# Kernel tuning notes

Measured on AMD Instinct MI355X. Metric: run time of the kernel, lower is better.

## Reference

```python
import jax, jax.numpy as jnp
import numpy as np

EPS_MASK = 1e-6   # clamp eps from DNN_Beamformer __init__
EPS_MVDR = 1e-15  # eps in get_mvdr_vector / psd normalization
SCALING = 2.0     # AttentionReference softmax scaling


def _psd(xs, mask):
    # xs: (B,F,C,T) complex, mask: (B,F,C,T) real -> psd: (B,F,C,C) complex
    m = mask.mean(axis=-2)                                   # (B,F,T)
    m = m / (m.sum(axis=-1, keepdims=True) + EPS_MVDR)
    # sum_t xs[c,t] * conj(xs[e,t]) * m[t], never materializing (B,F,T,C,C)
    return jnp.einsum('bfct,bfet,bft->bfce', xs, xs.conj(), m)


def _attention_reference(psd_in, mlp_w, mlp_b, gvec_w, gvec_b):
    # psd_in: (B,F,C,C) complex -> u: (B,C)
    C = psd_in.shape[-1]
    eye = jnp.eye(C, dtype=bool)
    psd = jnp.where(eye, 0.0, psd_in)                        # zero diagonal
    psd = psd.sum(axis=-1) / (C - 1)                         # (B,F,C)
    psd = jnp.swapaxes(psd, -1, -2)                          # (B,C,F)
    feat = jnp.sqrt(psd.real ** 2 + psd.imag ** 2)           # (B,C,F)
    h = jnp.tanh(feat @ mlp_w + mlp_b)                       # (B,C,att)
    e = (h @ gvec_w + gvec_b)[..., 0]                        # (B,C)
    return jax.nn.softmax(SCALING * e, axis=-1)


def _mvdr_vector(psd_s, psd_n, u):
    # psd_s, psd_n: (B,F,C,C) complex; u: (B,C) real -> ws: (B,F,C) complex
    C = psd_n.shape[-1]
    psd_n = psd_n + EPS_MVDR * jnp.eye(C, dtype=psd_n.dtype)
    numerator = jnp.linalg.solve(psd_n, psd_s)               # inv(psd_n) @ psd_s
    tr = jnp.trace(numerator, axis1=-2, axis2=-1)            # (B,F)
    ws = numerator / (tr[..., None, None] + EPS_MVDR)        # (B,F,C,C)
    return jnp.einsum('bfec,bc->bfe', ws, u.astype(ws.dtype))


def setup_inputs() -> dict:
    key = jax.random.key(0)
    ks = jax.random.split(key, 8)
    B, T, C, F, A = 8, 800, 8, 513, 320
    return {
        'data_real': jax.random.normal(ks[0], (B, T, C, F), jnp.float32),
        'data_imag': jax.random.normal(ks[1], (B, T, C, F), jnp.float32),
        'mask_speech': jax.random.uniform(ks[2], (B, F, C, T), jnp.float32),
        'mask_noise': jax.random.uniform(ks[3], (B, F, C, T), jnp.float32),
        'mlp_w': jax.random.normal(ks[4], (F, A), jnp.float32) / np.sqrt(F),
        'mlp_b': jnp.zeros((A,), jnp.float32),
        'gvec_w': jax.random.normal(ks[5], (A, 1), jnp.float32) / np.sqrt(A),
        'gvec_b': jnp.zeros((1,), jnp.float32),
        'ilens': jnp.full((8,), 800, dtype=jnp.int32),
    }


def reference(data_real, data_imag, mask_speech, mask_noise,
              mlp_w, mlp_b, gvec_w, gvec_b, ilens):
    # data: (B,T,C,F) -> permuted to (B,F,C,T) as in forward
    data = data_real + 1j * data_imag
    x = jnp.transpose(data, (0, 3, 2, 1))                    # (B,F,C,T)
    ms = jnp.maximum(mask_speech, EPS_MASK)
    mn = jnp.maximum(mask_noise, EPS_MASK)
    psd_s = _psd(x, ms)                                      # (B,F,C,C)
    psd_n = _psd(x, mn)                                      # (B,F,C,C)
    u = _attention_reference(psd_s, mlp_w, mlp_b, gvec_w, gvec_b)  # (B,C)
    ws = _mvdr_vector(psd_s, psd_n, u)                       # (B,F,C)
    enhanced = jnp.einsum('bfc,bfct->bft', ws.conj(), x)     # (B,F,T)
    enhanced = jnp.swapaxes(enhanced, -1, -2)                # (B,T,F)
    # return real/imag stacked so the output is a real tensor
    return jnp.stack([enhanced.real, enhanced.imag], axis=-1)
```

## Files before the change

kernel.cpp:

```cpp
#include <hip/hip_runtime.h>
#include <math.h>

#define NB 8
#define NT 800
#define NC 8
#define NF 513
#define NFT 9
#define NTC 50
#define TCHUNK 16
#define NE 146
#define NPAIR 36


__global__ __launch_bounds__(256)
void k_maskred(const float* __restrict__ ms, const float* __restrict__ mn,
               float* __restrict__ mrs, float* __restrict__ mrn) {
  __shared__ float ts[64][65];
  __shared__ float tn[64][65];
  const int ft = blockIdx.x, tt = blockIdx.y, b = blockIdx.z;
  const int f0 = ft * 64, t0 = tt * 64;
  const int tq = threadIdx.x & 15;
  const int fy = threadIdx.x >> 4;
  const int t = t0 + tq * 4;
  const bool tvalid = (t < NT);

#pragma unroll
  for (int p = 0; p < 4; p++) {
    const int fl = p * 16 + fy;
    const int f = f0 + fl;
    float4 as = make_float4(0.f, 0.f, 0.f, 0.f);
    float4 an = make_float4(0.f, 0.f, 0.f, 0.f);
    if (f < NF && tvalid) {
      const float* mbs = ms + (((size_t)b * NF + f) * NC) * NT + t;
      const float* mbn = mn + (((size_t)b * NF + f) * NC) * NT + t;
#pragma unroll
      for (int c = 0; c < NC; c++) {
        const float4 a = *(const float4*)(mbs + c * NT);
        as.x += fmaxf(a.x, 1e-6f); as.y += fmaxf(a.y, 1e-6f);
        as.z += fmaxf(a.z, 1e-6f); as.w += fmaxf(a.w, 1e-6f);
        const float4 q = *(const float4*)(mbn + c * NT);
        an.x += fmaxf(q.x, 1e-6f); an.y += fmaxf(q.y, 1e-6f);
        an.z += fmaxf(q.z, 1e-6f); an.w += fmaxf(q.w, 1e-6f);
      }
    }
    ts[fl][tq * 4 + 0] = as.x * 0.125f; ts[fl][tq * 4 + 1] = as.y * 0.125f;
    ts[fl][tq * 4 + 2] = as.z * 0.125f; ts[fl][tq * 4 + 3] = as.w * 0.125f;
    tn[fl][tq * 4 + 0] = an.x * 0.125f; tn[fl][tq * 4 + 1] = an.y * 0.125f;
    tn[fl][tq * 4 + 2] = an.z * 0.125f; tn[fl][tq * 4 + 3] = an.w * 0.125f;
  }
  __syncthreads();
  const int tx = threadIdx.x & 63, wy = threadIdx.x >> 6;
  for (int tl = wy; tl < 64; tl += 4) {
    const int tg = t0 + tl, f = f0 + tx;
    if (tg < NT && f < NF) {
      mrs[((size_t)b * NT + tg) * NF + f] = ts[tx][tl];
      mrn[((size_t)b * NT + tg) * NF + f] = tn[tx][tl];
    }
  }
}

__device__ __forceinline__ void accum_psd(const float* __restrict__ drb,
                                          const float* __restrict__ dib, int t,
                                          float m_s, float m_n,
                                          float* __restrict__ sr, float* __restrict__ si,
                                          float* __restrict__ nr, float* __restrict__ ni) {
  float xr[NC], xi[NC];
#pragma unroll
  for (int c = 0; c < NC; c++) {
    xr[c] = drb[(t * NC + c) * NF];
    xi[c] = dib[(t * NC + c) * NF];
  }
  int p = 0;
#pragma unroll
  for (int c = 0; c < NC; c++) {
#pragma unroll
    for (int e = c; e < NC; e++) {
      float pr = xr[c] * xr[e] + xi[c] * xi[e];
      float pi = xi[c] * xr[e] - xr[c] * xi[e];
      sr[p] += m_s * pr; si[p] += m_s * pi;
      nr[p] += m_n * pr; ni[p] += m_n * pi;
      p++;
    }
  }
}

__global__ __launch_bounds__(64, 2)
void k_psd(const float* __restrict__ dr, const float* __restrict__ di,
           const float* __restrict__ mrs, const float* __restrict__ mrn,
           float* __restrict__ comp) {
  const int fl = threadIdx.x;
  const int ft = blockIdx.x, b = blockIdx.y, tc = blockIdx.z;
  const int f = ft * 64 + fl;

  float sr[NPAIR], si[NPAIR], nr[NPAIR], ni[NPAIR];
#pragma unroll
  for (int p = 0; p < NPAIR; p++) { sr[p] = 0.f; si[p] = 0.f; nr[p] = 0.f; ni[p] = 0.f; }
  float Ss = 0.f, Sn = 0.f;

  if (f < NF) {
    const float* drb  = dr  + (size_t)b * NT * NC * NF + f;
    const float* dib  = di  + (size_t)b * NT * NC * NF + f;
    const float* mrsb = mrs + (size_t)b * NT * NF + f;
    const float* mrnb = mrn + (size_t)b * NT * NF + f;
    const int t0 = tc * TCHUNK;
    for (int tb = 0; tb < TCHUNK; tb += 2) {
      const int t = t0 + tb;
      const float ms0 = mrsb[(size_t)t * NF];
      const float ms1 = mrsb[(size_t)(t + 1) * NF];
      const float mn0 = mrnb[(size_t)t * NF];
      const float mn1 = mrnb[(size_t)(t + 1) * NF];
      Ss += ms0 + ms1; Sn += mn0 + mn1;
      accum_psd(drb, dib, t,     ms0, mn0, sr, si, nr, ni);
      accum_psd(drb, dib, t + 1, ms1, mn1, sr, si, nr, ni);
    }
  }

  float* out = comp + (((size_t)b * NFT + ft) * NE) * 64 + fl;
  if (f < NF) {
#pragma unroll
    for (int p = 0; p < NPAIR; p++) {
      unsafeAtomicAdd(&out[(2 * p) * 64], sr[p]);
      unsafeAtomicAdd(&out[(2 * p + 1) * 64], si[p]);
    }
#pragma unroll
    for (int p = 0; p < NPAIR; p++) {
      unsafeAtomicAdd(&out[(72 + 2 * p) * 64], nr[p]);
      unsafeAtomicAdd(&out[(72 + 2 * p + 1) * 64], ni[p]);
    }
    unsafeAtomicAdd(&out[144 * 64], Ss);
    unsafeAtomicAdd(&out[145 * 64], Sn);
  }
}

__global__ __launch_bounds__(320)
void k_attention(const float* __restrict__ comp,
                 const float* __restrict__ mlp_w, const float* __restrict__ mlp_b,
                 const float* __restrict__ gvec_w, const float* __restrict__ gvec_b,
                 float* __restrict__ e_buf) {
  __shared__ float feat[NF];
  __shared__ float wred[5];
  const int b = blockIdx.x >> 3, c = blockIdx.x & 7;
  const int tid = threadIdx.x;

  for (int f = tid; f < NF; f += 320) {
    const int ft = f >> 6, fl = f & 63;
    const float* base = comp + (((size_t)b * NFT + ft) * NE) * 64 + fl;
    float rs = 0.f, is = 0.f;
#pragma unroll
    for (int e = 0; e < NC; ++e) {
      if (e == c) continue;
      const int lo = (e < c) ? e : c, hi = (e < c) ? c : e;
      const int p = lo * 8 - (lo * (lo + 1)) / 2 + hi;
      rs += base[(2 * p) * 64];
      const float im = base[(2 * p + 1) * 64];
      is += (e > c) ? im : -im;
    }
    const float S = base[144 * 64];
    feat[f] = sqrtf(rs * rs + is * is) / (7.f * (S + 1e-15f));
  }
  __syncthreads();

  const int a = tid;
  float acc = mlp_b[a];
  for (int f = 0; f < NF; ++f) acc = fmaf(feat[f], mlp_w[f * 320 + a], acc);
  float contrib = tanhf(acc) * gvec_w[a];
#pragma unroll
  for (int off = 32; off > 0; off >>= 1) contrib += __shfl_down(contrib, off);
  if ((tid & 63) == 0) wred[tid >> 6] = contrib;
  __syncthreads();
  if (tid == 0) {
    float s = gvec_b[0];
#pragma unroll
    for (int w = 0; w < 5; ++w) s += wred[w];
    e_buf[blockIdx.x] = s;
  }
}

__global__ __launch_bounds__(64)
void k_solve(const float* __restrict__ comp, const float* __restrict__ e_buf,
             float* __restrict__ wsvec) {
  const int lane = threadIdx.x;
  const int c = lane & 7, fsub = lane >> 3;
  const int b = blockIdx.y;
  const int f = blockIdx.x * 8 + fsub;
  if (f >= NF) return;
  const int ft = f >> 6, fl = f & 63;
  const float* base = comp + (((size_t)b * NFT + ft) * NE) * 64 + fl;

  float Ar[8][8], Ai[8][8];
#pragma unroll
  for (int j = 0; j < 8; j++) {
#pragma unroll
    for (int i = j; i < 8; i++) {
      const int p = j * 8 - (j * (j + 1)) / 2 + i;
      Ar[i][j] = base[(72 + 2 * p) * 64];
      Ai[i][j] = (i == j) ? 0.f : -base[(72 + 2 * p + 1) * 64];
    }
  }
#pragma unroll
  for (int i = 0; i < 8; i++) Ar[i][i] += 1e-15f;

  float dinv[8];
#pragma unroll
  for (int k = 0; k < 8; k++) {
    const float d = sqrtf(fmaxf(Ar[k][k], 1e-30f));
    const float id = 1.f / d;
    dinv[k] = id;
#pragma unroll
    for (int i = k + 1; i < 8; i++) { Ar[i][k] *= id; Ai[i][k] *= id; }
#pragma unroll
    for (int j = k + 1; j < 8; j++) {
#pragma unroll
      for (int i = j; i < 8; i++) {
        Ar[i][j] -= Ar[i][k] * Ar[j][k] + Ai[i][k] * Ai[j][k];
        Ai[i][j] -= Ai[i][k] * Ar[j][k] - Ar[i][k] * Ai[j][k];
      }
    }
  }

  float syr[8], syi[8];
#pragma unroll
  for (int e = 0; e < 8; e++) {
    const int lo = (e < c) ? e : c, hi = (e < c) ? c : e;
    const int p = lo * 8 - (lo * (lo + 1)) / 2 + hi;
    syr[e] = base[(2 * p) * 64];
    const float im = base[(2 * p + 1) * 64];
    syi[e] = (e <= c) ? im : -im;
  }
  float yr[8], yi[8];
#pragma unroll
  for (int i = 0; i < 8; i++) {
    float ar = syr[i], ai = syi[i];
#pragma unroll
    for (int m = 0; m < 8; m++) {
      if (m < i) {
        ar -= Ar[i][m] * yr[m] - Ai[i][m] * yi[m];
        ai -= Ar[i][m] * yi[m] + Ai[i][m] * yr[m];
      }
    }
    yr[i] = ar * dinv[i]; yi[i] = ai * dinv[i];
  }
  float zr[8], zi[8];
#pragma unroll
  for (int i = 7; i >= 0; i--) {
    float ar = yr[i], ai = yi[i];
#pragma unroll
    for (int m = 0; m < 8; m++) {
      if (m > i) {
        ar -= Ar[m][i] * zr[m] + Ai[m][i] * zi[m];
        ai -= Ar[m][i] * zi[m] - Ai[m][i] * zr[m];
      }
    }
    zr[i] = ar * dinv[i]; zi[i] = ai * dinv[i];
  }

  float ev[8], mx = -1e30f;
#pragma unroll
  for (int j = 0; j < 8; j++) { ev[j] = 2.f * e_buf[b * 8 + j]; mx = fmaxf(mx, ev[j]); }
  float ssum = 0.f;
#pragma unroll
  for (int j = 0; j < 8; j++) ssum += expf(ev[j] - mx);
  const float uc = expf(ev[c] - mx) / ssum;

  float trr = zr[c], tri = zi[c];
  float wr[8], wi[8];
#pragma unroll
  for (int e = 0; e < 8; e++) { wr[e] = zr[e] * uc; wi[e] = zi[e] * uc; }
#pragma unroll
  for (int m = 1; m <= 4; m <<= 1) {
    trr += __shfl_xor(trr, m); tri += __shfl_xor(tri, m);
#pragma unroll
    for (int e = 0; e < 8; e++) {
      wr[e] += __shfl_xor(wr[e], m);
      wi[e] += __shfl_xor(wi[e], m);
    }
  }

  const float denr = trr + 1e-15f, deni = tri;
  const float inv = 1.f / (denr * denr + deni * deni);
  float2* wv = (float2*)wsvec + ((size_t)b * NF + f) * 8;
  wv[c] = make_float2((wr[c] * denr + wi[c] * deni) * inv,
                      (wi[c] * denr - wr[c] * deni) * inv);
}

__global__ __launch_bounds__(64)
void k_apply(const float* __restrict__ dr, const float* __restrict__ di,
             const float* __restrict__ wsvec, float* __restrict__ out) {
  const int ft = blockIdx.x, b = blockIdx.y, tt = blockIdx.z;
  const int f = ft * 64 + threadIdx.x;
  if (f >= NF) return;
  float wr[8], wi[8];
  const float2* wv = (const float2*)wsvec + ((size_t)b * NF + f) * 8;
#pragma unroll
  for (int c = 0; c < 8; c++) { float2 w = wv[c]; wr[c] = w.x; wi[c] = w.y; }
  const float* drb = dr + (size_t)b * NT * NC * NF + f;
  const float* dib = di + (size_t)b * NT * NC * NF + f;
  float2* ob = (float2*)out + (size_t)b * NT * NF + f;
  const int t1 = tt * 8 + 8;
  for (int t = tt * 8; t < t1; ++t) {
    float re = 0.f, im = 0.f;
#pragma unroll
    for (int c = 0; c < 8; c++) {
      const float xr = drb[(t * NC + c) * NF];
      const float xi = dib[(t * NC + c) * NF];
      re += wr[c] * xr + wi[c] * xi;
      im += wr[c] * xi - wi[c] * xr;
    }
    ob[(size_t)t * NF] = make_float2(re, im);
  }
}

extern "C" void kernel_launch(void* const* d_in, const int* in_sizes, int n_in,
                              void* d_out, int out_size, void* d_ws, size_t ws_size,
                              hipStream_t stream) {
  const float* dr     = (const float*)d_in[0];
  const float* di     = (const float*)d_in[1];
  const float* msk_s  = (const float*)d_in[2];
  const float* msk_n  = (const float*)d_in[3];
  const float* mlp_w  = (const float*)d_in[4];
  const float* mlp_b  = (const float*)d_in[5];
  const float* gvec_w = (const float*)d_in[6];
  const float* gvec_b = (const float*)d_in[7];

  float* mrs   = (float*)d_ws;
  float* mrn   = mrs + (size_t)NB * NT * NF;
  float* comp  = mrn + (size_t)NB * NT * NF;
  float* e_buf = comp + (size_t)NB * NFT * NE * 64;
  float* wsvec = e_buf + 64;
  float* out   = (float*)d_out;

  hipMemsetAsync(comp, 0, (size_t)NB * NFT * NE * 64 * sizeof(float), stream);
  k_maskred<<<dim3(NFT, 13, NB), 256, 0, stream>>>(msk_s, msk_n, mrs, mrn);
  k_psd<<<dim3(NFT, NB, NTC), 64, 0, stream>>>(dr, di, mrs, mrn, comp);
  k_attention<<<64, 320, 0, stream>>>(comp, mlp_w, mlp_b, gvec_w, gvec_b, e_buf);
  k_solve<<<dim3(65, NB), 64, 0, stream>>>(comp, e_buf, wsvec);
  k_apply<<<dim3(NFT, NB, 100), 64, 0, stream>>>(dr, di, wsvec, out);
}
```

Baseline: 570.9 us.

## Reduce PSD partials in shared memory before global atomics

The PSD kernel now runs four 64-lane waves per block, each covering a 20-frame slice of an 80-frame chunk, and combines their partial sums in a shared-memory buffer before a single round of global atomic adds. This cuts global atomic traffic to the accumulation buffer roughly fivefold by cutting the number of time chunks. In exchange it adds LDS atomics, two block barriers, a 37 KB shared buffer that may limit occupancy, and non-coalesced zero-fill work. The launch-bounds hint moves to 256 threads with four blocks per CU, which may also change register allocation for the 146-float accumulator set.

```diff
diff --git a/kernel.cpp b/kernel.cpp
--- a/kernel.cpp
+++ b/kernel.cpp
@@ -6,8 +6,9 @@
 #define NC 8
 #define NF 513
 #define NFT 9
-#define NTC 50
-#define TCHUNK 16
+#define NTC 10
+#define TCHUNK 80
+#define TW 20
 #define NE 146
 #define NPAIR 36
 
@@ -84,11 +85,14 @@
   }
 }
 
-__global__ __launch_bounds__(64, 2)
+__global__ __launch_bounds__(256, 4)
 void k_psd(const float* __restrict__ dr, const float* __restrict__ di,
            const float* __restrict__ mrs, const float* __restrict__ mrn,
            float* __restrict__ comp) {
-  const int fl = threadIdx.x;
+  __shared__ float red[NE][64];
+  const int tid = threadIdx.x;
+  const int fl = tid & 63;
+  const int w  = tid >> 6;
   const int ft = blockIdx.x, b = blockIdx.y, tc = blockIdx.z;
   const int f = ft * 64 + fl;
 
@@ -102,8 +106,8 @@
     const float* dib  = di  + (size_t)b * NT * NC * NF + f;
     const float* mrsb = mrs + (size_t)b * NT * NF + f;
     const float* mrnb = mrn + (size_t)b * NT * NF + f;
-    const int t0 = tc * TCHUNK;
-    for (int tb = 0; tb < TCHUNK; tb += 2) {
+    const int t0 = tc * TCHUNK + w * TW;
+    for (int tb = 0; tb < TW; tb += 2) {
       const int t = t0 + tb;
       const float ms0 = mrsb[(size_t)t * NF];
       const float ms1 = mrsb[(size_t)(t + 1) * NF];
@@ -115,21 +119,26 @@
     }
   }
 
-  float* out = comp + (((size_t)b * NFT + ft) * NE) * 64 + fl;
-  if (f < NF) {
-#pragma unroll
-    for (int p = 0; p < NPAIR; p++) {
-      unsafeAtomicAdd(&out[(2 * p) * 64], sr[p]);
-      unsafeAtomicAdd(&out[(2 * p + 1) * 64], si[p]);
-    }
-#pragma unroll
-    for (int p = 0; p < NPAIR; p++) {
-      unsafeAtomicAdd(&out[(72 + 2 * p) * 64], nr[p]);
-      unsafeAtomicAdd(&out[(72 + 2 * p + 1) * 64], ni[p]);
-    }
-    unsafeAtomicAdd(&out[144 * 64], Ss);
-    unsafeAtomicAdd(&out[145 * 64], Sn);
-  }
+  for (int i = tid; i < NE * 64; i += 256) ((float*)red)[i] = 0.f;
+  __syncthreads();
+
+#pragma unroll
+  for (int p = 0; p < NPAIR; p++) {
+    atomicAdd(&red[2 * p][fl], sr[p]);
+    atomicAdd(&red[2 * p + 1][fl], si[p]);
+  }
+#pragma unroll
+  for (int p = 0; p < NPAIR; p++) {
+    atomicAdd(&red[72 + 2 * p][fl], nr[p]);
+    atomicAdd(&red[72 + 2 * p + 1][fl], ni[p]);
+  }
+  atomicAdd(&red[144][fl], Ss);
+  atomicAdd(&red[145][fl], Sn);
+  __syncthreads();
+
+  float* outb = comp + ((size_t)(b * NFT + ft) * NE) * 64;
+  for (int i = tid; i < NE * 64; i += 256)
+    unsafeAtomicAdd(&outb[i], ((const float*)red)[i]);
 }
 
 __global__ __launch_bounds__(320)
@@ -331,7 +340,7 @@
 
   hipMemsetAsync(comp, 0, (size_t)NB * NFT * NE * 64 * sizeof(float), stream);
   k_maskred<<<dim3(NFT, 13, NB), 256, 0, stream>>>(msk_s, msk_n, mrs, mrn);
-  k_psd<<<dim3(NFT, NB, NTC), 64, 0, stream>>>(dr, di, mrs, mrn, comp);
+  k_psd<<<dim3(NFT, NB, NTC), 256, 0, stream>>>(dr, di, mrs, mrn, comp);
   k_attention<<<64, 320, 0, stream>>>(comp, mlp_w, mlp_b, gvec_w, gvec_b, e_buf);
   k_solve<<<dim3(65, NB), 64, 0, stream>>>(comp, e_buf, wsvec);
   k_apply<<<dim3(NFT, NB, 100), 64, 0, stream>>>(dr, di, wsvec, out);
```

Result: slower. 897.3 us (+57.2%).

## Double-buffer PSD tiles in LDS and split channel pairs across four waves

Applied to the files above, without the earlier changes.

Rewrites the PSD accumulation kernel to use 256-thread blocks. Each of the four waves owns 9 of the 36 channel pairs, which cuts per-thread register accumulators from 146 to about 38. Data and mask tiles are staged into LDS with global_load_lds, double-buffered so the next time slice loads while the current one computes. Time chunks grow from 16 to 40, which cuts the number of atomic flushes. The cost is extra barriers and LDS traffic, plus fewer blocks along time.

```diff
diff --git a/kernel.cpp b/kernel.cpp
--- a/kernel.cpp
+++ b/kernel.cpp
@@ -6,11 +6,25 @@
 #define NC 8
 #define NF 513
 #define NFT 9
-#define NTC 50
-#define TCHUNK 16
+#define NTC 20
+#define TCHUNK 40
+#define TS 4
+#define NSTG (TCHUNK / TS)
 #define NE 146
 #define NPAIR 36
-
+#define STRIDE_BUF (72 * 64)
+
+
+constexpr int PCt[4][9] = {
+    {0, 1, 2, 3, 4, 5, 6, 7, 0},
+    {0, 1, 2, 3, 4, 5, 6, 0, 1},
+    {0, 1, 2, 3, 4, 5, 0, 1, 2},
+    {0, 1, 2, 3, 4, 0, 1, 2, 3}};
+constexpr int PEt[4][9] = {
+    {0, 1, 2, 3, 4, 5, 6, 7, 7},
+    {1, 2, 3, 4, 5, 6, 7, 6, 7},
+    {2, 3, 4, 5, 6, 7, 5, 6, 7},
+    {3, 4, 5, 6, 7, 4, 5, 6, 7}};
 
 __global__ __launch_bounds__(256)
 void k_maskred(const float* __restrict__ ms, const float* __restrict__ mn,
@@ -59,74 +73,131 @@
   }
 }
 
-__device__ __forceinline__ void accum_psd(const float* __restrict__ drb,
-                                          const float* __restrict__ dib, int t,
-                                          float m_s, float m_n,
-                                          float* __restrict__ sr, float* __restrict__ si,
-                                          float* __restrict__ nr, float* __restrict__ ni) {
-  float xr[NC], xi[NC];
-#pragma unroll
-  for (int c = 0; c < NC; c++) {
-    xr[c] = drb[(t * NC + c) * NF];
-    xi[c] = dib[(t * NC + c) * NF];
-  }
-  int p = 0;
-#pragma unroll
-  for (int c = 0; c < NC; c++) {
-#pragma unroll
-    for (int e = c; e < NC; e++) {
-      float pr = xr[c] * xr[e] + xi[c] * xi[e];
-      float pi = xi[c] * xr[e] - xr[c] * xi[e];
-      sr[p] += m_s * pr; si[p] += m_s * pi;
-      nr[p] += m_n * pr; ni[p] += m_n * pi;
-      p++;
-    }
-  }
-}
-
-__global__ __launch_bounds__(64, 2)
+__device__ __forceinline__ void stage_tile(const float* __restrict__ drb,
+                                           const float* __restrict__ dib,
+                                           const float* __restrict__ mrsb,
+                                           const float* __restrict__ mrnb,
+                                           float* buf, int tbase, int w, int fglob) {
+#pragma unroll
+  for (int r = 0; r < 18; ++r) {
+    const int row = r * 4 + w;
+    const float* src;
+    if (r < 16) {
+      const int t = row >> 4, c = (row >> 1) & 7;
+      const float* base = (row & 1) ? dib : drb;
+      src = base + ((size_t)(tbase + t) * NC + c) * NF + fglob;
+    } else {
+      const int t = (row - 64) >> 1;
+      const float* base = (row & 1) ? mrnb : mrsb;
+      src = base + (size_t)(tbase + t) * NF + fglob;
+    }
+    __builtin_amdgcn_global_load_lds(
+        (const __attribute__((address_space(1))) void*)src,
+        (__attribute__((address_space(3))) void*)(buf + row * 64),
+        4, 0, 0);
+  }
+}
+
+template <int W>
+__device__ __forceinline__ void psd_compute_tile(const float* __restrict__ buf,
+                                                 int fl,
+                                                 float sr[9], float si[9],
+                                                 float nr[9], float ni[9],
+                                                 float& Ss, float& Sn) {
+#pragma unroll
+  for (int t = 0; t < TS; ++t) {
+    float xr[8], xi[8];
+#pragma unroll
+    for (int c = 0; c < 8; ++c) {
+      xr[c] = buf[(t * 16 + c * 2 + 0) * 64 + fl];
+      xi[c] = buf[(t * 16 + c * 2 + 1) * 64 + fl];
+    }
+    const float ms = buf[(64 + t * 2 + 0) * 64 + fl];
+    const float mn = buf[(64 + t * 2 + 1) * 64 + fl];
+    if (W == 0) { Ss += ms; Sn += mn; }
+#pragma unroll
+    for (int k = 0; k < 9; ++k) {
+      const int c = PCt[W][k], e = PEt[W][k];
+      const float pr = xr[c] * xr[e] + xi[c] * xi[e];
+      sr[k] += ms * pr; nr[k] += mn * pr;
+      if (c != e) {
+        const float pi = xi[c] * xr[e] - xr[c] * xi[e];
+        si[k] += ms * pi; ni[k] += mn * pi;
+      }
+    }
+  }
+}
+
+template <int W>
+__device__ __forceinline__ void psd_sweep(float* __restrict__ out,
+                                          const float sr[9], const float si[9],
+                                          const float nr[9], const float ni[9]) {
+#pragma unroll
+  for (int k = 0; k < 9; ++k) {
+    const int c = PCt[W][k], e = PEt[W][k];
+    const int p = c * 8 - (c * (c + 1)) / 2 + e;
+    unsafeAtomicAdd(&out[(2 * p) * 64], sr[k]);
+    unsafeAtomicAdd(&out[(72 + 2 * p) * 64], nr[k]);
+    if (c != e) {
+      unsafeAtomicAdd(&out[(2 * p + 1) * 64], si[k]);
+      unsafeAtomicAdd(&out[(72 + 2 * p + 1) * 64], ni[k]);
+    }
+  }
+}
+
+__global__ __launch_bounds__(256, 4)
 void k_psd(const float* __restrict__ dr, const float* __restrict__ di,
            const float* __restrict__ mrs, const float* __restrict__ mrn,
            float* __restrict__ comp) {
-  const int fl = threadIdx.x;
+  __shared__ float lds[2 * STRIDE_BUF];
+  const int tid = threadIdx.x;
+  const int fl = tid & 63;
+  const int w  = tid >> 6;
   const int ft = blockIdx.x, b = blockIdx.y, tc = blockIdx.z;
-  const int f = ft * 64 + fl;
-
-  float sr[NPAIR], si[NPAIR], nr[NPAIR], ni[NPAIR];
-#pragma unroll
-  for (int p = 0; p < NPAIR; p++) { sr[p] = 0.f; si[p] = 0.f; nr[p] = 0.f; ni[p] = 0.f; }
+  const int fglob = min(ft * 64 + fl, NF - 1);
+  const int t0 = tc * TCHUNK;
+
+  const float* drb  = dr  + (size_t)b * NT * NC * NF;
+  const float* dib  = di  + (size_t)b * NT * NC * NF;
+  const float* mrsb = mrs + (size_t)b * NT * NF;
+  const float* mrnb = mrn + (size_t)b * NT * NF;
+
+  float sr[9], si[9], nr[9], ni[9];
+#pragma unroll
+  for (int k = 0; k < 9; ++k) { sr[k] = 0.f; si[k] = 0.f; nr[k] = 0.f; ni[k] = 0.f; }
   float Ss = 0.f, Sn = 0.f;
 
-  if (f < NF) {
-    const float* drb  = dr  + (size_t)b * NT * NC * NF + f;
-    const float* dib  = di  + (size_t)b * NT * NC * NF + f;
-    const float* mrsb = mrs + (size_t)b * NT * NF + f;
-    const float* mrnb = mrn + (size_t)b * NT * NF + f;
-    const int t0 = tc * TCHUNK;
-    for (int tb = 0; tb < TCHUNK; tb += 2) {
-      const int t = t0 + tb;
-      const float ms0 = mrsb[(size_t)t * NF];
-      const float ms1 = mrsb[(size_t)(t + 1) * NF];
-      const float mn0 = mrnb[(size_t)t * NF];
-      const float mn1 = mrnb[(size_t)(t + 1) * NF];
-      Ss += ms0 + ms1; Sn += mn0 + mn1;
-      accum_psd(drb, dib, t,     ms0, mn0, sr, si, nr, ni);
-      accum_psd(drb, dib, t + 1, ms1, mn1, sr, si, nr, ni);
-    }
-  }
-
-  float* out = comp + (((size_t)b * NFT + ft) * NE) * 64 + fl;
-  if (f < NF) {
-#pragma unroll
-    for (int p = 0; p < NPAIR; p++) {
-      unsafeAtomicAdd(&out[(2 * p) * 64], sr[p]);
-      unsafeAtomicAdd(&out[(2 * p + 1) * 64], si[p]);
-    }
-#pragma unroll
-    for (int p = 0; p < NPAIR; p++) {
-      unsafeAtomicAdd(&out[(72 + 2 * p) * 64], nr[p]);
-      unsafeAtomicAdd(&out[(72 + 2 * p + 1) * 64], ni[p]);
-    }
+  stage_tile(drb, dib, mrsb, mrnb, &lds[0], t0, w, fglob);
+  asm volatile("s_waitcnt vmcnt(0)" ::: "memory");
+  __syncthreads();
+
+  int cur = 0;
+  for (int s = 0; s < NSTG; ++s) {
+    if (s + 1 < NSTG)
+      stage_tile(drb, dib, mrsb, mrnb, &lds[(cur ^ 1) * STRIDE_BUF],
+                 t0 + (s + 1) * TS, w, fglob);
+    const float* buf = &lds[cur * STRIDE_BUF];
+    switch (w) {
+      case 0: psd_compute_tile<0>(buf, fl, sr, si, nr, ni, Ss, Sn); break;
+      case 1: psd_compute_tile<1>(buf, fl, sr, si, nr, ni, Ss, Sn); break;
+      case 2: psd_compute_tile<2>(buf, fl, sr, si, nr, ni, Ss, Sn); break;
+      default: psd_compute_tile<3>(buf, fl, sr, si, nr, ni, Ss, Sn); break;
+    }
+    if (s + 1 < NSTG) {
+      asm volatile("s_waitcnt vmcnt(0)" ::: "memory");
+      __syncthreads();
+      cur ^= 1;
+    }
+  }
+
+  float* out = comp + ((size_t)(b * NFT + ft) * NE) * 64 + fl;
+  switch (w) {
+    case 0: psd_sweep<0>(out, sr, si, nr, ni); break;
+    case 1: psd_sweep<1>(out, sr, si, nr, ni); break;
+    case 2: psd_sweep<2>(out, sr, si, nr, ni); break;
+    default: psd_sweep<3>(out, sr, si, nr, ni); break;
+  }
+  if (w == 0) {
     unsafeAtomicAdd(&out[144 * 64], Ss);
     unsafeAtomicAdd(&out[145 * 64], Sn);
   }
@@ -331,7 +402,7 @@
 
   hipMemsetAsync(comp, 0, (size_t)NB * NFT * NE * 64 * sizeof(float), stream);
   k_maskred<<<dim3(NFT, 13, NB), 256, 0, stream>>>(msk_s, msk_n, mrs, mrn);
-  k_psd<<<dim3(NFT, NB, NTC), 64, 0, stream>>>(dr, di, mrs, mrn, comp);
+  k_psd<<<dim3(NFT, NB, NTC), 256, 0, stream>>>(dr, di, mrs, mrn, comp);
   k_attention<<<64, 320, 0, stream>>>(comp, mlp_w, mlp_b, gvec_w, gvec_b, e_buf);
   k_solve<<<dim3(65, NB), 64, 0, stream>>>(comp, e_buf, wsvec);
   k_apply<<<dim3(NFT, NB, 100), 64, 0, stream>>>(dr, di, wsvec, out);
```

Result: slower. 848.5 us (+48.6%).
